# Kernel tuning notes

Hardware: AMD Instinct MI355X
Metric: run time of the kernel (lower is better)

The kernel has to match this reference:

```python
import jax, jax.numpy as jnp
import numpy as np

# Binarize (sign) with straight-through estimator, matching the BNN-style
# BinarizeConv2d which replaces .data in-place (identity gradient path).
@jax.custom_vjp
def binarize(x):
    return jnp.where(x >= 0, 1.0, -1.0).astype(x.dtype)

def _bin_fwd(x):
    return binarize(x), None

def _bin_bwd(_, g):
    return (g,)

binarize.defvjp(_bin_fwd, _bin_bwd)

def conv2d(x, w, pad):
    # x: NCHW, w: OIHW, stride 1, symmetric 'same' padding for odd kernels
    return jax.lax.conv_general_dilated(
        x, w, window_strides=(1, 1), padding=[(pad, pad), (pad, pad)],
        dimension_numbers=("NCHW", "OIHW", "NCHW"))

def batchnorm2d(x, gamma, beta, eps=1e-5):
    # training-mode BatchNorm2d: batch statistics over (N, H, W)
    mean = jnp.mean(x, axis=(0, 2, 3), keepdims=True)
    var = jnp.var(x, axis=(0, 2, 3), keepdims=True)
    inv = gamma[None, :, None, None] * jax.lax.rsqrt(var + eps)
    return (x - mean) * inv + beta[None, :, None, None]

def leaky_relu(x, slope=0.5):
    return jnp.where(x >= 0, x, slope * x)

def setup_inputs() -> dict:
    key = jax.random.key(0)
    ks = jax.random.split(key, 4)
    B, H, W = 16, 256, 256
    x = jax.random.normal(ks[0], (B, 1, H, W), dtype=jnp.float32)
    w1 = jax.random.normal(ks[1], (128, 1, 7, 7), dtype=jnp.float32) * 0.1
    w2 = jax.random.normal(ks[2], (64, 128, 1, 1), dtype=jnp.float32) * 0.1
    w3 = jax.random.normal(ks[3], (1, 64, 5, 5), dtype=jnp.float32) * 0.05
    g1 = jnp.ones((128,), jnp.float32)
    b1 = jnp.zeros((128,), jnp.float32)
    g2 = jnp.ones((64,), jnp.float32)
    b2 = jnp.zeros((64,), jnp.float32)
    return {"x": x, "w1": w1, "g1": g1, "b1": b1,
            "w2": w2, "g2": g2, "b2": b2, "w3": w3}

def reference(x, w1, g1, b1, w2, g2, b2, w3):
    # layer1: binarized conv (in=1 channel != 3 -> input also binarized) + BN + LeakyReLU(0.5)
    h = conv2d(binarize(x), binarize(w1), pad=3)
    h = leaky_relu(batchnorm2d(h, g1, b1))
    # layer2: binarized 1x1 conv + BN + LeakyReLU(0.5)
    h = conv2d(binarize(h), binarize(w2), pad=0)
    h = leaky_relu(batchnorm2d(h, g2, b2))
    # layer3: plain full-precision 5x5 conv, no bias
    return conv2d(h, w3, pad=2)
```

## Files before the change

kernel.cpp:

```cpp
#include <hip/hip_runtime.h>
#include <cstdint>
#include <cstddef>
#include <climits>


#define NPIX_PER_CH (16.0 * 256.0 * 256.0)
#define PLANE_BYTES 67584
#define ROW_BYTES   264
#define FXSCALE     262144.0f
#define FXINV       3.814697265625e-06f

typedef _Float16 half2_t __attribute__((ext_vector_type(2)));

#if __has_builtin(__builtin_amdgcn_fdot2)
__device__ __forceinline__ float DOT2(half2_t a, half2_t b, float c) {
    return __builtin_amdgcn_fdot2(a, b, c, false);
}
#else
__device__ __forceinline__ float DOT2(half2_t a, half2_t b, float c) {
    return fmaf((float)a[0], (float)b[0], fmaf((float)a[1], (float)b[1], c));
}
#endif

__device__ __forceinline__ uint32_t pk_f16(float lo, float hi) {
#if __has_builtin(__builtin_amdgcn_cvt_pkrtz)
    auto h = __builtin_amdgcn_cvt_pkrtz(lo, hi);
    return __builtin_bit_cast(uint32_t, h);
#else
    half2_t h; h[0] = (_Float16)lo; h[1] = (_Float16)hi;
    return __builtin_bit_cast(uint32_t, h);
#endif
}
#define H2(u) __builtin_bit_cast(half2_t, (uint32_t)(u))

struct WS {
    int8_t*   h2s;
    uint64_t* xbits;
    uint64_t* wb1;
    uint64_t* w2lo;
    uint64_t* w2hi;
    long long* st1;
    long long* st2;
    int*      K1;
    unsigned long long* flipm;
    float* a2; float* c2;
    uint32_t* wtab;
};

static inline WS carve(void* d_ws) {
    WS w;
    uint8_t* p = (uint8_t*)d_ws;
    w.h2s   = (int8_t*)p;              p += (size_t)16 * 64 * PLANE_BYTES;
    w.xbits = (uint64_t*)p;            p += (size_t)16 * 256 * 6 * 8;
    w.wb1   = (uint64_t*)p;            p += 128 * 8;
    w.w2lo  = (uint64_t*)p;            p += 64 * 8;
    w.w2hi  = (uint64_t*)p;            p += 64 * 8;
    w.st1   = (long long*)p;           p += 256 * 8;
    w.st2   = (long long*)p;           p += 128 * 8;
    w.K1    = (int*)p;                 p += 128 * 4;
    w.flipm = (unsigned long long*)p;  p += 2 * 8;
    w.a2    = (float*)p;               p += 64 * 4;
    w.c2    = (float*)p;               p += 64 * 4;
    w.wtab  = (uint32_t*)p;            p += 64 * 32 * 4;
    return w;
}

__global__ __launch_bounds__(256) void k_pack_x(const float* __restrict__ x,
                                                uint64_t* __restrict__ xbits) {
    int rowId = blockIdx.x * 4 + (threadIdx.x >> 6);
    int lane  = threadIdx.x & 63;
    const float* row = x + (size_t)rowId * 256;
    uint64_t b0 = __ballot(row[0 * 64 + lane] < 0.0f);
    uint64_t b1 = __ballot(row[1 * 64 + lane] < 0.0f);
    uint64_t b2 = __ballot(row[2 * 64 + lane] < 0.0f);
    uint64_t b3 = __ballot(row[3 * 64 + lane] < 0.0f);
    if (lane == 0) {
        uint64_t* o = xbits + (size_t)rowId * 6;
        o[0] = b0 << 8;
        o[1] = (b0 >> 56) | (b1 << 8);
        o[2] = (b1 >> 56) | (b2 << 8);
        o[3] = (b2 >> 56) | (b3 << 8);
        o[4] = b3 >> 56;
        o[5] = 0;
    }
}

__global__ void k_pack_w(const float* __restrict__ w1, const float* __restrict__ w2,
                         uint64_t* __restrict__ wb1, uint64_t* __restrict__ w2lo,
                         uint64_t* __restrict__ w2hi,
                         long long* __restrict__ st1, long long* __restrict__ st2) {
    int t = threadIdx.x;
    if (t < 128) {
        uint64_t b = 0;
        for (int k = 0; k < 49; ++k)
            if (w1[t * 49 + k] < 0.0f) b |= (1ull << k);
        wb1[t] = b;
    } else if (t < 192) {
        int o = t - 128;
        uint64_t lo = 0, hi = 0;
        for (int c = 0; c < 64; ++c) if (w2[o * 128 + c]      < 0.0f) lo |= (1ull << c);
        for (int c = 0; c < 64; ++c) if (w2[o * 128 + 64 + c] < 0.0f) hi |= (1ull << c);
        w2lo[o] = lo; w2hi[o] = hi;
    }
    st1[t] = 0;
    if (t < 128) st2[t] = 0;
}

__device__ inline void build_window(const uint64_t* __restrict__ xb_img, int y, int x,
                                    uint64_t& sbits, uint64_t& vmask) {
    int bitpos = x + 5;
    int w  = bitpos >> 6;
    int sh = bitpos & 63;
    int lo = 3 - x;   if (lo < 0) lo = 0;
    int hi = 258 - x; if (hi > 6) hi = 6;
    uint64_t hm = ((1ull << (hi - lo + 1)) - 1ull) << lo;
    sbits = 0; vmask = 0;
    #pragma unroll
    for (int dy = 0; dy < 7; ++dy) {
        int yy = y - 3 + dy;
        if (yy < 0 || yy > 255) continue;
        const uint64_t* r = xb_img + (size_t)yy * 6;
        uint64_t wA = r[w], wB = r[w + 1];
        uint64_t bits = wA >> sh;
        if (sh) bits |= wB << (64 - sh);
        bits &= 0x7Full;
        sbits |= bits << (7 * dy);
        vmask |= hm   << (7 * dy);
    }
}

__global__ __launch_bounds__(256) void k_stats1(const uint64_t* __restrict__ xbits,
                                                const uint64_t* __restrict__ wb1g,
                                                long long* __restrict__ st1) {
    __shared__ uint64_t sb[256];
    __shared__ uint64_t vm[256];
    __shared__ int       rs[128];
    __shared__ int       rq[128];
    int t = threadIdx.x;
    int c = t & 127, half = t >> 7;
    uint64_t wb = wb1g[c];
    int sum = 0;
    int sumsq = 0;
    for (int row = blockIdx.x; row < 4096; row += gridDim.x) {
        int n = row >> 8, y = row & 255;
        const uint64_t* xb_img = xbits + (size_t)n * 256 * 6;
        uint64_t s, v;
        build_window(xb_img, y, t, s, v);
        sb[t] = s; vm[t] = v;
        __syncthreads();
        int base = half << 7;
        #pragma unroll 4
        for (int p = 0; p < 128; ++p) {
            uint64_t ss = sb[base + p], vv = vm[base + p];
            uint64_t d = (ss ^ wb) & vv;
            int h = __popcll(vv) - 2 * __popcll(d);
            sum += h;
            sumsq += h * h;
        }
        __syncthreads();
    }
    if (half == 1) { rs[c] = sum; rq[c] = sumsq; }
    __syncthreads();
    if (half == 0) {
        long long S = (long long)sum + rs[c];
        long long Q = (long long)sumsq + rq[c];
        atomicAdd((unsigned long long*)&st1[c],       (unsigned long long)S);
        atomicAdd((unsigned long long*)&st1[128 + c], (unsigned long long)Q);
    }
}

__global__ void k_fin1(const long long* __restrict__ st1,
                       const float* __restrict__ g1, const float* __restrict__ b1,
                       int* __restrict__ K1, unsigned long long* __restrict__ flipm) {
    int c = threadIdx.x;
    double mean = (double)st1[c] / NPIX_PER_CH;
    double var  = (double)st1[128 + c] / NPIX_PER_CH - mean * mean;
    double a = (double)g1[c] / sqrt(var + 1e-5);
    double cst = (double)b1[c] - mean * a;
    int K; int flip = 0;
    if (a > 0.0) {
        double v = -cst / a;
        v = fmin(fmax(v, -100.0), 100.0);
        K = (int)ceil(v);
    } else if (a < 0.0) {
        double v = -cst / a;
        v = fmin(fmax(v, -100.0), 100.0);
        K = (int)floor(v) + 1; flip = 1;
    } else {
        K = INT_MIN; flip = (cst < 0.0) ? 1 : 0;
    }
    K1[c] = K;
    unsigned long long m = __ballot(flip != 0);
    if ((c & 63) == 0) flipm[c >> 6] = m;
}

__global__ __launch_bounds__(256) void k_conv2(const uint64_t* __restrict__ xbits,
                                               const uint64_t* __restrict__ wb1g,
                                               const int* __restrict__ K1g,
                                               const unsigned long long* __restrict__ flipm,
                                               const uint64_t* __restrict__ w2log,
                                               const uint64_t* __restrict__ w2hig,
                                               int8_t* __restrict__ h2s) {
    __shared__ uint64_t wb1s[128];
    __shared__ int      K1s[128];
    __shared__ uint64_t w2l[64], w2h[64];
    int t = threadIdx.x;
    if (t < 128) { wb1s[t] = wb1g[t]; K1s[t] = K1g[t]; }
    else if (t < 192) { int o = t - 128; w2l[o] = w2log[o]; w2h[o] = w2hig[o]; }
    __syncthreads();

    int idx = blockIdx.x * 256 + t;
    int n = idx >> 16, rem = idx & 65535;
    int y = rem >> 8, x = rem & 255;
    const uint64_t* xb_img = xbits + (size_t)n * 256 * 6;
    uint64_t sbits, vmask;
    build_window(xb_img, y, x, sbits, vmask);
    int nv = __popcll(vmask);

    uint64_t blo = 0, bhi = 0;
    #pragma unroll 8
    for (int cc = 0; cc < 64; ++cc) {
        uint64_t d = (sbits ^ wb1s[cc]) & vmask;
        int h = nv - 2 * __popcll(d);
        blo |= (uint64_t)(h < K1s[cc]) << cc;
    }
    #pragma unroll 8
    for (int cc = 0; cc < 64; ++cc) {
        uint64_t d = (sbits ^ wb1s[64 + cc]) & vmask;
        int h = nv - 2 * __popcll(d);
        bhi |= (uint64_t)(h < K1s[64 + cc]) << cc;
    }
    blo ^= flipm[0];
    bhi ^= flipm[1];

    size_t base = (size_t)(n * 64) * PLANE_BYTES + (size_t)y * ROW_BYTES;
    #pragma unroll 8
    for (int o = 0; o < 64; ++o) {
        int m = __popcll(blo ^ w2l[o]) + __popcll(bhi ^ w2h[o]);
        h2s[base + (size_t)o * PLANE_BYTES + 2 + x] = (int8_t)(64 - m);
    }
    if (x == 0) {
        #pragma unroll 8
        for (int o = 0; o < 64; ++o)
            *(short*)(h2s + base + (size_t)o * PLANE_BYTES) = 0;
    }
    if (x == 255) {
        #pragma unroll 8
        for (int o = 0; o < 64; ++o) {
            int8_t* r = h2s + base + (size_t)o * PLANE_BYTES;
            *(short*)(r + 258) = 0;
            *(int*)(r + 260) = 0;
        }
    }
}

__global__ __launch_bounds__(256) void k_stats2(const int8_t* __restrict__ h2s,
                                                long long* __restrict__ st2) {
    int plane = blockIdx.x;
    int o = plane & 63;
    int t = threadIdx.x;
    const int4* p = (const int4*)(h2s + (size_t)plane * PLANE_BYTES);
    int sum = 0, sumsq = 0;
    for (int si = t; si < 4224; si += 256) {
        int4 v4 = p[si];
        int wv[4] = {v4.x, v4.y, v4.z, v4.w};
        #pragma unroll
        for (int j = 0; j < 4; ++j) {
            #pragma unroll
            for (int k = 0; k < 4; ++k) {
                int b = (int)(int8_t)((unsigned)wv[j] >> (8 * k));
                sum += b;
                sumsq += b * b;
            }
        }
    }
    for (int off = 32; off; off >>= 1) {
        sum   += __shfl_down(sum, off);
        sumsq += __shfl_down(sumsq, off);
    }
    __shared__ int ws1[4], ws2[4];
    int wid = t >> 6;
    if ((t & 63) == 0) { ws1[wid] = sum; ws2[wid] = sumsq; }
    __syncthreads();
    if (t == 0) {
        long long S = 0, Q = 0;
        for (int i = 0; i < 4; ++i) { S += ws1[i]; Q += ws2[i]; }
        atomicAdd((unsigned long long*)&st2[o],      (unsigned long long)S);
        atomicAdd((unsigned long long*)&st2[64 + o], (unsigned long long)Q);
    }
}

__global__ void k_fin2(const long long* __restrict__ st2,
                       const float* __restrict__ g2, const float* __restrict__ b2,
                       const float* __restrict__ w3,
                       float* __restrict__ a2, float* __restrict__ c2,
                       uint32_t* __restrict__ wtab) {
    int o = threadIdx.x;
    double mean = 2.0 * (double)st2[o] / NPIX_PER_CH;
    double msq  = 4.0 * (double)st2[64 + o] / NPIX_PER_CH;
    double var  = msq - mean * mean;
    double inv  = (double)g2[o] / sqrt(var + 1e-5);
    a2[o] = (float)(2.0 * inv);
    c2[o] = (float)((double)b2[o] - mean * inv);

    uint32_t* wp = wtab + o * 32;
    #pragma unroll
    for (int dy = 0; dy < 5; ++dy) {
        float w0 = w3[o * 25 + dy * 5 + 0];
        float w1 = w3[o * 25 + dy * 5 + 1];
        float w2v = w3[o * 25 + dy * 5 + 2];
        float w3v = w3[o * 25 + dy * 5 + 3];
        float w4 = w3[o * 25 + dy * 5 + 4];
        half2_t h;
        h[0] = (_Float16)w0;  h[1] = (_Float16)w1;  wp[dy*6+0] = __builtin_bit_cast(uint32_t, h);
        h[0] = (_Float16)w2v; h[1] = (_Float16)w3v; wp[dy*6+1] = __builtin_bit_cast(uint32_t, h);
        h[0] = (_Float16)w4;  h[1] = (_Float16)0.f; wp[dy*6+2] = __builtin_bit_cast(uint32_t, h);
        h[0] = (_Float16)0.f; h[1] = (_Float16)w0;  wp[dy*6+3] = __builtin_bit_cast(uint32_t, h);
        h[0] = (_Float16)w1;  h[1] = (_Float16)w2v; wp[dy*6+4] = __builtin_bit_cast(uint32_t, h);
        h[0] = (_Float16)w3v; h[1] = (_Float16)w4;  wp[dy*6+5] = __builtin_bit_cast(uint32_t, h);
    }
    wp[30] = 0; wp[31] = 0;
}

__global__ __launch_bounds__(256) void k_zero3(int4* __restrict__ o) {
    int i = blockIdx.x * 256 + threadIdx.x;
    #pragma unroll
    for (int j = 0; j < 4; ++j)
        o[(size_t)i * 4 + j] = make_int4(0, 0, 0, 0);
}

__global__ __launch_bounds__(256, 4) void k_conv3(const int8_t* __restrict__ h2s,
                                                  const float* __restrict__ a2g,
                                                  const float* __restrict__ c2g,
                                                  const uint32_t* __restrict__ wtab,
                                                  int* __restrict__ outi) {
    __shared__ uint16_t lds[4 * 36 * 72];
    __shared__ float sA2[32], sC2[32];
    int t = threadIdx.x;
    int bid = blockIdx.x;
    int cg   = bid >> 9;
    int rest = bid & 511;
    int n  = rest >> 5;
    int yt = (rest >> 2) & 7;
    int xt = rest & 3;
    int ty0 = yt * 32, tx0 = xt * 64;
    int cgbase = cg * 32;
    if (t < 32) { sA2[t] = a2g[cgbase + t]; sC2[t] = c2g[cgbase + t]; }

    int ty = t >> 4, tx = t & 15;
    int n64 = n * 64;

    float acc[2][4] = {{0.f,0.f,0.f,0.f},{0.f,0.f,0.f,0.f}};

    for (int kk = 0; kk < 8; ++kk) {
        __syncthreads();
        for (int si = t; si < 2448; si += 256) {
            int cl  = si / 612;
            int rem = si - cl * 612;
            int row = rem / 17;
            int q   = rem - row * 17;
            int gy  = ty0 - 2 + row;
            int lc  = 4 * kk + cl;
            float a = sA2[lc], c = sC2[lc];
            uint32_t u0 = 0, u1 = 0;
            if ((unsigned)gy < 256u) {
                int v = *(const int*)(h2s + (size_t)(n64 + cgbase + lc) * PLANE_BYTES
                                          + (size_t)gy * ROW_BYTES + tx0 + q * 4);
                float z0 = fmaf(a, (float)(int)(int8_t)(v),        c);
                float z1 = fmaf(a, (float)(int)(int8_t)(v >> 8),   c);
                float z2 = fmaf(a, (float)(int)(int8_t)(v >> 16),  c);
                float z3 = fmaf(a, (float)(int)(int8_t)(v >> 24),  c);
                z0 = fmaxf(z0, 0.5f * z0);
                z1 = fmaxf(z1, 0.5f * z1);
                z2 = fmaxf(z2, 0.5f * z2);
                z3 = fmaxf(z3, 0.5f * z3);
                u0 = pk_f16(z0, z1);
                u1 = pk_f16(z2, z3);
            }
            uint2 wv = {u0, u1};
            *(uint2*)(lds + cl * 2592 + row * 72 + q * 4) = wv;
        }
        __syncthreads();

        #pragma unroll
        for (int cl = 0; cl < 4; ++cl) {
            const uint32_t* wp = wtab + (size_t)(cgbase + 4 * kk + cl) * 32;
            const uint16_t* base = lds + cl * 2592 + (2 * ty) * 72 + 4 * tx;
            #pragma unroll
            for (int rr = 0; rr < 6; ++rr) {
                uint2 A = *(const uint2*)(base + rr * 72);
                uint2 B = *(const uint2*)(base + rr * 72 + 4);
                half2_t W0 = H2(A.x), W1 = H2(A.y), W2 = H2(B.x), W3 = H2(B.y);
                #pragma unroll
                for (int dyp = rr - 1; dyp <= rr; ++dyp) {
                    if (dyp < 0 || dyp > 4) continue;
                    int r = rr - dyp;
                    const uint32_t* wd = wp + dyp * 6;
                    acc[r][0] = DOT2(W0, H2(wd[0]), DOT2(W1, H2(wd[1]), DOT2(W2, H2(wd[2]), acc[r][0])));
                    acc[r][1] = DOT2(W0, H2(wd[3]), DOT2(W1, H2(wd[4]), DOT2(W2, H2(wd[5]), acc[r][1])));
                    acc[r][2] = DOT2(W1, H2(wd[0]), DOT2(W2, H2(wd[1]), DOT2(W3, H2(wd[2]), acc[r][2])));
                    acc[r][3] = DOT2(W1, H2(wd[3]), DOT2(W2, H2(wd[4]), DOT2(W3, H2(wd[5]), acc[r][3])));
                }
            }
        }
    }

    int ox = tx0 + 4 * tx;
    #pragma unroll
    for (int r = 0; r < 2; ++r) {
        int oy = ty0 + 2 * ty + r;
        size_t o = (size_t)n * 65536 + (size_t)oy * 256 + ox;
        #pragma unroll
        for (int j = 0; j < 4; ++j) {
            int q = __float2int_rn(acc[r][j] * FXSCALE);
            atomicAdd(outi + o + j, q);
        }
    }
}

__global__ __launch_bounds__(256) void k_fin3(int* __restrict__ o) {
    int i = blockIdx.x * 256 + threadIdx.x;
    int4 v = ((const int4*)o)[i];
    float4 f = {v.x * FXINV, v.y * FXINV, v.z * FXINV, v.w * FXINV};
    ((float4*)o)[i] = f;
}

extern "C" void kernel_launch(void* const* d_in, const int* in_sizes, int n_in,
                              void* d_out, int out_size, void* d_ws, size_t ws_size,
                              hipStream_t stream) {
    const float* x  = (const float*)d_in[0];
    const float* w1 = (const float*)d_in[1];
    const float* g1 = (const float*)d_in[2];
    const float* b1 = (const float*)d_in[3];
    const float* w2 = (const float*)d_in[4];
    const float* g2 = (const float*)d_in[5];
    const float* b2 = (const float*)d_in[6];
    const float* w3 = (const float*)d_in[7];

    WS ws = carve(d_ws);

    k_zero3<<<256, 256, 0, stream>>>((int4*)d_out);
    k_pack_x<<<1024, 256, 0, stream>>>(x, ws.xbits);
    k_pack_w<<<1, 256, 0, stream>>>(w1, w2, ws.wb1, ws.w2lo, ws.w2hi, ws.st1, ws.st2);
    k_stats1<<<1024, 256, 0, stream>>>(ws.xbits, ws.wb1, ws.st1);
    k_fin1<<<1, 128, 0, stream>>>(ws.st1, g1, b1, ws.K1, ws.flipm);
    k_conv2<<<4096, 256, 0, stream>>>(ws.xbits, ws.wb1, ws.K1, ws.flipm,
                                      ws.w2lo, ws.w2hi, ws.h2s);
    k_stats2<<<1024, 256, 0, stream>>>(ws.h2s, ws.st2);
    k_fin2<<<1, 64, 0, stream>>>(ws.st2, g2, b2, w3, ws.a2, ws.c2, ws.wtab);
    k_conv3<<<1024, 256, 0, stream>>>(ws.h2s, ws.a2, ws.c2, ws.wtab, (int*)d_out);
    k_fin3<<<1024, 256, 0, stream>>>((int*)d_out);
}
```

Before: 244.4 us.

## Fuse layer-2 statistics into conv2 and reorganize conv2 per-row with packed stores

The k_stats2 pass is removed and the channel sum and sum-of-squares for layer 2 are computed inside k_conv2, which now handles one image row per block. Binarized layer-1 bits are staged in shared memory, so each thread writes coalesced 4-byte words of one output channel instead of scattered single bytes. The stats1 loop skips the validity mask for interior pixels, and conv3 loads all LDS rows before computing. Together these cut a full re-read of the int8 intermediate and reduce uncoalesced global writes, at the cost of extra LDS traffic and atomics per block.

```diff
diff --git a/kernel.cpp b/kernel.cpp
--- a/kernel.cpp
+++ b/kernel.cpp
@@ -41,7 +41,7 @@
     uint64_t* w2hi;
     long long* st1;
     long long* st2;
-    int*      K1;
+    uint4*    pk1;
     unsigned long long* flipm;
     float* a2; float* c2;
     uint32_t* wtab;
@@ -57,7 +57,7 @@
     w.w2hi  = (uint64_t*)p;            p += 64 * 8;
     w.st1   = (long long*)p;           p += 256 * 8;
     w.st2   = (long long*)p;           p += 128 * 8;
-    w.K1    = (int*)p;                 p += 128 * 4;
+    w.pk1   = (uint4*)p;               p += 128 * 16;
     w.flipm = (unsigned long long*)p;  p += 2 * 8;
     w.a2    = (float*)p;               p += 64 * 4;
     w.c2    = (float*)p;               p += 64 * 4;
@@ -134,8 +134,8 @@
                                                 long long* __restrict__ st1) {
     __shared__ uint64_t sb[256];
     __shared__ uint64_t vm[256];
-    __shared__ int       rs[128];
-    __shared__ int       rq[128];
+    __shared__ int rs[128];
+    __shared__ int rq[128];
     int t = threadIdx.x;
     int c = t & 127, half = t >> 7;
     uint64_t wb = wb1g[c];
@@ -149,13 +149,26 @@
         sb[t] = s; vm[t] = v;
         __syncthreads();
         int base = half << 7;
-        #pragma unroll 4
-        for (int p = 0; p < 128; ++p) {
-            uint64_t ss = sb[base + p], vv = vm[base + p];
-            uint64_t d = (ss ^ wb) & vv;
+        auto edge = [&](int p) {
+            uint64_t vv = vm[base + p];
+            uint64_t d = (sb[base + p] ^ wb) & vv;
             int h = __popcll(vv) - 2 * __popcll(d);
-            sum += h;
-            sumsq += h * h;
+            sum += h; sumsq += h * h;
+        };
+        if (y >= 3 && y <= 252) {
+            int lo = (half == 0) ? 3 : 0;
+            int hi = (half == 0) ? 128 : 125;
+            for (int p = 0; p < lo; ++p) edge(p);
+            #pragma unroll 4
+            for (int p = lo; p < hi; ++p) {
+                uint64_t d = sb[base + p] ^ wb;
+                int h = 49 - 2 * __popcll(d);
+                sum += h; sumsq += h * h;
+            }
+            for (int p = hi; p < 128; ++p) edge(p);
+        } else {
+            #pragma unroll 4
+            for (int p = 0; p < 128; ++p) edge(p);
         }
         __syncthreads();
     }
@@ -171,7 +184,8 @@
 
 __global__ void k_fin1(const long long* __restrict__ st1,
                        const float* __restrict__ g1, const float* __restrict__ b1,
-                       int* __restrict__ K1, unsigned long long* __restrict__ flipm) {
+                       const uint64_t* __restrict__ wb1,
+                       uint4* __restrict__ pk1, unsigned long long* __restrict__ flipm) {
     int c = threadIdx.x;
     double mean = (double)st1[c] / NPIX_PER_CH;
     double var  = (double)st1[128 + c] / NPIX_PER_CH - mean * mean;
@@ -189,104 +203,117 @@
     } else {
         K = INT_MIN; flip = (cst < 0.0) ? 1 : 0;
     }
-    K1[c] = K;
+    uint64_t wb = wb1[c];
+    pk1[c] = make_uint4((uint32_t)wb, (uint32_t)(wb >> 32), (uint32_t)K, 0u);
     unsigned long long m = __ballot(flip != 0);
     if ((c & 63) == 0) flipm[c >> 6] = m;
 }
 
 __global__ __launch_bounds__(256) void k_conv2(const uint64_t* __restrict__ xbits,
-                                               const uint64_t* __restrict__ wb1g,
-                                               const int* __restrict__ K1g,
+                                               const uint4* __restrict__ pk1,
                                                const unsigned long long* __restrict__ flipm,
                                                const uint64_t* __restrict__ w2log,
                                                const uint64_t* __restrict__ w2hig,
-                                               int8_t* __restrict__ h2s) {
-    __shared__ uint64_t wb1s[128];
-    __shared__ int      K1s[128];
-    __shared__ uint64_t w2l[64], w2h[64];
+                                               int8_t* __restrict__ h2s,
+                                               long long* __restrict__ st2) {
+    __shared__ uint4 s_pk[128];
+    __shared__ uint4 sB[256];
     int t = threadIdx.x;
-    if (t < 128) { wb1s[t] = wb1g[t]; K1s[t] = K1g[t]; }
-    else if (t < 192) { int o = t - 128; w2l[o] = w2log[o]; w2h[o] = w2hig[o]; }
-    __syncthreads();
-
-    int idx = blockIdx.x * 256 + t;
-    int n = idx >> 16, rem = idx & 65535;
-    int y = rem >> 8, x = rem & 255;
+    if (t < 128) s_pk[t] = pk1[t];
+    unsigned long long f0 = flipm[0], f1 = flipm[1];
+    int blk = blockIdx.x;
+    int n = blk >> 8, y = blk & 255;
     const uint64_t* xb_img = xbits + (size_t)n * 256 * 6;
     uint64_t sbits, vmask;
-    build_window(xb_img, y, x, sbits, vmask);
+    build_window(xb_img, y, t, sbits, vmask);
     int nv = __popcll(vmask);
+    __syncthreads();
 
     uint64_t blo = 0, bhi = 0;
     #pragma unroll 8
     for (int cc = 0; cc < 64; ++cc) {
-        uint64_t d = (sbits ^ wb1s[cc]) & vmask;
+        uint4 pk = s_pk[cc];
+        uint64_t wb = ((uint64_t)pk.y << 32) | pk.x;
+        uint64_t d = (sbits ^ wb) & vmask;
         int h = nv - 2 * __popcll(d);
-        blo |= (uint64_t)(h < K1s[cc]) << cc;
+        blo |= (uint64_t)(h < (int)pk.z) << cc;
     }
     #pragma unroll 8
     for (int cc = 0; cc < 64; ++cc) {
-        uint64_t d = (sbits ^ wb1s[64 + cc]) & vmask;
+        uint4 pk = s_pk[64 + cc];
+        uint64_t wb = ((uint64_t)pk.y << 32) | pk.x;
+        uint64_t d = (sbits ^ wb) & vmask;
         int h = nv - 2 * __popcll(d);
-        bhi |= (uint64_t)(h < K1s[64 + cc]) << cc;
-    }
-    blo ^= flipm[0];
-    bhi ^= flipm[1];
-
-    size_t base = (size_t)(n * 64) * PLANE_BYTES + (size_t)y * ROW_BYTES;
-    #pragma unroll 8
-    for (int o = 0; o < 64; ++o) {
-        int m = __popcll(blo ^ w2l[o]) + __popcll(bhi ^ w2h[o]);
-        h2s[base + (size_t)o * PLANE_BYTES + 2 + x] = (int8_t)(64 - m);
-    }
-    if (x == 0) {
-        #pragma unroll 8
-        for (int o = 0; o < 64; ++o)
-            *(short*)(h2s + base + (size_t)o * PLANE_BYTES) = 0;
-    }
-    if (x == 255) {
-        #pragma unroll 8
-        for (int o = 0; o < 64; ++o) {
-            int8_t* r = h2s + base + (size_t)o * PLANE_BYTES;
-            *(short*)(r + 258) = 0;
-            *(int*)(r + 260) = 0;
-        }
-    }
-}
-
-__global__ __launch_bounds__(256) void k_stats2(const int8_t* __restrict__ h2s,
-                                                long long* __restrict__ st2) {
-    int plane = blockIdx.x;
-    int o = plane & 63;
-    int t = threadIdx.x;
-    const int4* p = (const int4*)(h2s + (size_t)plane * PLANE_BYTES);
-    int sum = 0, sumsq = 0;
-    for (int si = t; si < 4224; si += 256) {
-        int4 v4 = p[si];
-        int wv[4] = {v4.x, v4.y, v4.z, v4.w};
+        bhi |= (uint64_t)(h < (int)pk.z) << cc;
+    }
+    blo ^= f0; bhi ^= f1;
+    sB[t] = make_uint4((uint32_t)blo, (uint32_t)(blo >> 32),
+                       (uint32_t)bhi, (uint32_t)(bhi >> 32));
+    __syncthreads();
+
+    int o = t >> 2, q = t & 3;
+    uint64_t wl = w2log[o], wh = w2hig[o];
+    uint32_t wl0 = (uint32_t)wl, wl1 = (uint32_t)(wl >> 32);
+    uint32_t wh0 = (uint32_t)wh, wh1 = (uint32_t)(wh >> 32);
+    uint8_t* rowp = (uint8_t*)h2s + (size_t)(n * 64 + o) * PLANE_BYTES
+                                  + (size_t)y * ROW_BYTES;
+    int sum = 0, sq = 0;
+
+    auto pxval = [&](int x) -> int {
+        uint4 p = sB[x];
+        int m = __popc(p.x ^ wl0) + __popc(p.y ^ wl1)
+              + __popc(p.z ^ wh0) + __popc(p.w ^ wh1);
+        return 64 - m;
+    };
+
+    {
+        int byte = 4 * q;
+        uint32_t w = 0;
         #pragma unroll
-        for (int j = 0; j < 4; ++j) {
+        for (int bb = 0; bb < 4; ++bb) {
+            int x = byte + bb - 2;
+            if (x >= 0) {
+                int v = pxval(x);
+                sum += v; sq += v * v;
+                w |= (uint32_t)(uint8_t)(int8_t)v << (8 * bb);
+            }
+        }
+        *(uint32_t*)(rowp + byte) = w;
+    }
+    #pragma unroll 5
+    for (int i = 1; i < 16; ++i) {
+        int byte = 16 * i + 4 * q;
+        uint32_t w = 0;
+        #pragma unroll
+        for (int bb = 0; bb < 4; ++bb) {
+            int v = pxval(byte + bb - 2);
+            sum += v; sq += v * v;
+            w |= (uint32_t)(uint8_t)(int8_t)v << (8 * bb);
+        }
+        *(uint32_t*)(rowp + byte) = w;
+    }
+    {
+        int byte = 256 + 4 * q;
+        if (byte < 264) {
+            uint32_t w = 0;
             #pragma unroll
-            for (int k = 0; k < 4; ++k) {
-                int b = (int)(int8_t)((unsigned)wv[j] >> (8 * k));
-                sum += b;
-                sumsq += b * b;
-            }
-        }
-    }
-    for (int off = 32; off; off >>= 1) {
-        sum   += __shfl_down(sum, off);
-        sumsq += __shfl_down(sumsq, off);
-    }
-    __shared__ int ws1[4], ws2[4];
-    int wid = t >> 6;
-    if ((t & 63) == 0) { ws1[wid] = sum; ws2[wid] = sumsq; }
-    __syncthreads();
-    if (t == 0) {
-        long long S = 0, Q = 0;
-        for (int i = 0; i < 4; ++i) { S += ws1[i]; Q += ws2[i]; }
-        atomicAdd((unsigned long long*)&st2[o],      (unsigned long long)S);
-        atomicAdd((unsigned long long*)&st2[64 + o], (unsigned long long)Q);
+            for (int bb = 0; bb < 4; ++bb) {
+                int x = byte + bb - 2;
+                if (x < 256) {
+                    int v = pxval(x);
+                    sum += v; sq += v * v;
+                    w |= (uint32_t)(uint8_t)(int8_t)v << (8 * bb);
+                }
+            }
+            *(uint32_t*)(rowp + byte) = w;
+        }
+    }
+
+    sum += __shfl_xor(sum, 1); sum += __shfl_xor(sum, 2);
+    sq  += __shfl_xor(sq, 1);  sq  += __shfl_xor(sq, 2);
+    if (q == 0) {
+        atomicAdd((unsigned long long*)&st2[o],      (unsigned long long)(long long)sum);
+        atomicAdd((unsigned long long*)&st2[64 + o], (unsigned long long)(long long)sq);
     }
 }
 
@@ -386,11 +413,16 @@
         for (int cl = 0; cl < 4; ++cl) {
             const uint32_t* wp = wtab + (size_t)(cgbase + 4 * kk + cl) * 32;
             const uint16_t* base = lds + cl * 2592 + (2 * ty) * 72 + 4 * tx;
+            uint2 A[6], B[6];
             #pragma unroll
             for (int rr = 0; rr < 6; ++rr) {
-                uint2 A = *(const uint2*)(base + rr * 72);
-                uint2 B = *(const uint2*)(base + rr * 72 + 4);
-                half2_t W0 = H2(A.x), W1 = H2(A.y), W2 = H2(B.x), W3 = H2(B.y);
+                A[rr] = *(const uint2*)(base + rr * 72);
+                B[rr] = *(const uint2*)(base + rr * 72 + 4);
+            }
+            #pragma unroll
+            for (int rr = 0; rr < 6; ++rr) {
+                half2_t W0 = H2(A[rr].x), W1 = H2(A[rr].y);
+                half2_t W2 = H2(B[rr].x), W3 = H2(B[rr].y);
                 #pragma unroll
                 for (int dyp = rr - 1; dyp <= rr; ++dyp) {
                     if (dyp < 0 || dyp > 4) continue;
@@ -443,10 +475,9 @@
     k_pack_x<<<1024, 256, 0, stream>>>(x, ws.xbits);
     k_pack_w<<<1, 256, 0, stream>>>(w1, w2, ws.wb1, ws.w2lo, ws.w2hi, ws.st1, ws.st2);
     k_stats1<<<1024, 256, 0, stream>>>(ws.xbits, ws.wb1, ws.st1);
-    k_fin1<<<1, 128, 0, stream>>>(ws.st1, g1, b1, ws.K1, ws.flipm);
-    k_conv2<<<4096, 256, 0, stream>>>(ws.xbits, ws.wb1, ws.K1, ws.flipm,
-                                      ws.w2lo, ws.w2hi, ws.h2s);
-    k_stats2<<<1024, 256, 0, stream>>>(ws.h2s, ws.st2);
+    k_fin1<<<1, 128, 0, stream>>>(ws.st1, g1, b1, ws.wb1, ws.pk1, ws.flipm);
+    k_conv2<<<4096, 256, 0, stream>>>(ws.xbits, ws.pk1, ws.flipm,
+                                      ws.w2lo, ws.w2hi, ws.h2s, ws.st2);
     k_fin2<<<1, 64, 0, stream>>>(ws.st2, g2, b2, w3, ws.a2, ws.c2, ws.wtab);
     k_conv3<<<1024, 256, 0, stream>>>(ws.h2s, ws.a2, ws.c2, ws.wtab, (int*)d_out);
     k_fin3<<<1024, 256, 0, stream>>>((int*)d_out);
```

Measured after the change: 274.2 us. +12.2%, slower.

## Split conv3 channel groups finer, batch LDS loads, fast-path interior stats1

Applied to the files above, without the earlier changes.

k_conv3 now splits the 64 input channels into four groups of 16 instead of two groups of 32, doubling the grid to 2048 blocks. Each block runs half as many channel iterations, and more blocks add their partial sums into the output atomically. Inside the inner loop all six LDS row loads are issued before the dot products, so their latency can overlap. In k_stats1, interior rows and columns skip the validity-mask popcount by using the constant 49, at the cost of extra branching and more atomic traffic on the output.

```diff
diff --git a/kernel.cpp b/kernel.cpp
--- a/kernel.cpp
+++ b/kernel.cpp
@@ -134,8 +134,8 @@
                                                 long long* __restrict__ st1) {
     __shared__ uint64_t sb[256];
     __shared__ uint64_t vm[256];
-    __shared__ int       rs[128];
-    __shared__ int       rq[128];
+    __shared__ int rs[128];
+    __shared__ int rq[128];
     int t = threadIdx.x;
     int c = t & 127, half = t >> 7;
     uint64_t wb = wb1g[c];
@@ -149,13 +149,26 @@
         sb[t] = s; vm[t] = v;
         __syncthreads();
         int base = half << 7;
-        #pragma unroll 4
-        for (int p = 0; p < 128; ++p) {
-            uint64_t ss = sb[base + p], vv = vm[base + p];
-            uint64_t d = (ss ^ wb) & vv;
+        auto edge = [&](int p) {
+            uint64_t vv = vm[base + p];
+            uint64_t d = (sb[base + p] ^ wb) & vv;
             int h = __popcll(vv) - 2 * __popcll(d);
-            sum += h;
-            sumsq += h * h;
+            sum += h; sumsq += h * h;
+        };
+        if (y >= 3 && y <= 252) {
+            int lo = (half == 0) ? 3 : 0;
+            int hi = (half == 0) ? 128 : 125;
+            for (int p = 0; p < lo; ++p) edge(p);
+            #pragma unroll 4
+            for (int p = lo; p < hi; ++p) {
+                uint64_t d = sb[base + p] ^ wb;
+                int h = 49 - 2 * __popcll(d);
+                sum += h; sumsq += h * h;
+            }
+            for (int p = hi; p < 128; ++p) edge(p);
+        } else {
+            #pragma unroll 4
+            for (int p = 0; p < 128; ++p) edge(p);
         }
         __syncthreads();
     }
@@ -335,7 +348,7 @@
                                                   const uint32_t* __restrict__ wtab,
                                                   int* __restrict__ outi) {
     __shared__ uint16_t lds[4 * 36 * 72];
-    __shared__ float sA2[32], sC2[32];
+    __shared__ float sA2[16], sC2[16];
     int t = threadIdx.x;
     int bid = blockIdx.x;
     int cg   = bid >> 9;
@@ -344,15 +357,15 @@
     int yt = (rest >> 2) & 7;
     int xt = rest & 3;
     int ty0 = yt * 32, tx0 = xt * 64;
-    int cgbase = cg * 32;
-    if (t < 32) { sA2[t] = a2g[cgbase + t]; sC2[t] = c2g[cgbase + t]; }
+    int cgbase = cg * 16;
+    if (t < 16) { sA2[t] = a2g[cgbase + t]; sC2[t] = c2g[cgbase + t]; }
 
     int ty = t >> 4, tx = t & 15;
     int n64 = n * 64;
 
     float acc[2][4] = {{0.f,0.f,0.f,0.f},{0.f,0.f,0.f,0.f}};
 
-    for (int kk = 0; kk < 8; ++kk) {
+    for (int kk = 0; kk < 4; ++kk) {
         __syncthreads();
         for (int si = t; si < 2448; si += 256) {
             int cl  = si / 612;
@@ -386,11 +399,16 @@
         for (int cl = 0; cl < 4; ++cl) {
             const uint32_t* wp = wtab + (size_t)(cgbase + 4 * kk + cl) * 32;
             const uint16_t* base = lds + cl * 2592 + (2 * ty) * 72 + 4 * tx;
+            uint2 A[6], B[6];
             #pragma unroll
             for (int rr = 0; rr < 6; ++rr) {
-                uint2 A = *(const uint2*)(base + rr * 72);
-                uint2 B = *(const uint2*)(base + rr * 72 + 4);
-                half2_t W0 = H2(A.x), W1 = H2(A.y), W2 = H2(B.x), W3 = H2(B.y);
+                A[rr] = *(const uint2*)(base + rr * 72);
+                B[rr] = *(const uint2*)(base + rr * 72 + 4);
+            }
+            #pragma unroll
+            for (int rr = 0; rr < 6; ++rr) {
+                half2_t W0 = H2(A[rr].x), W1 = H2(A[rr].y);
+                half2_t W2 = H2(B[rr].x), W3 = H2(B[rr].y);
                 #pragma unroll
                 for (int dyp = rr - 1; dyp <= rr; ++dyp) {
                     if (dyp < 0 || dyp > 4) continue;
@@ -448,6 +466,6 @@
                                       ws.w2lo, ws.w2hi, ws.h2s);
     k_stats2<<<1024, 256, 0, stream>>>(ws.h2s, ws.st2);
     k_fin2<<<1, 64, 0, stream>>>(ws.st2, g2, b2, w3, ws.a2, ws.c2, ws.wtab);
-    k_conv3<<<1024, 256, 0, stream>>>(ws.h2s, ws.a2, ws.c2, ws.wtab, (int*)d_out);
+    k_conv3<<<2048, 256, 0, stream>>>(ws.h2s, ws.a2, ws.c2, ws.wtab, (int*)d_out);
     k_fin3<<<1024, 256, 0, stream>>>((int*)d_out);
 }
```

Measured after the change: 244.1 us. About the same (-0.1%).
